# Kernel optimization log

Measured on AMD Instinct MI355X. Metric: run time of the kernel, lower is better.

Reference implementation:

```python
import jax, jax.numpy as jnp
import numpy as np

KERNEL = 7
PAD = 3
STRIDE = 1
DIL = 1
HEADS = 8
OUT_CH = 256


def _unfold(x, k, pad, stride, dil):
    # x: (B, C, H, W) -> (B, C*k*k, Ho, Wo); channel ordering (C, kh, kw),
    # matching torch.nn.Unfold's channel-major layout.
    return jax.lax.conv_general_dilated_patches(
        x, filter_shape=(k, k), window_strides=(stride, stride),
        padding=((pad, pad), (pad, pad)), rhs_dilation=(dil, dil))


def _conv1x1(x, w, b):
    # 1x1 conv == per-pixel matmul. w: (O, C), b: (O,)
    return jnp.einsum('bchw,oc->bohw', x, w) + b[None, :, None, None]


def setup_inputs() -> dict:
    key = jax.random.key(0)
    ks = jax.random.split(key, 11)
    B, C, H, W = 2, 256, 64, 64
    f = lambda k, sh: jax.random.normal(k, sh, dtype=jnp.float32)
    ws = 1.0 / np.sqrt(C).astype(np.float32)
    return dict(
        queries=f(ks[0], (B, C, H, W)),
        keys=f(ks[1], (B, C, H, W)),
        values=f(ks[2], (B, C, H, W)),
        wq=f(ks[3], (OUT_CH, C)) * ws, bq=f(ks[4], (OUT_CH,)) * 0.01,
        wk=f(ks[5], (OUT_CH, C)) * ws, bk=f(ks[6], (OUT_CH,)) * 0.01,
        wv=f(ks[7], (OUT_CH, C)) * ws, bv=f(ks[8], (OUT_CH,)) * 0.01,
        wo=f(ks[9], (OUT_CH, OUT_CH)) * ws, bo=f(ks[10], (OUT_CH,)) * 0.01,
    )


def reference(queries, keys, values, wq, bq, wk, bk, wv, bv, wo, bo):
    B = values.shape[0]
    d = OUT_CH // HEADS
    K2 = KERNEL * KERNEL
    q = _conv1x1(queries, wq, bq)
    k = _conv1x1(keys, wk, bk)
    v = _conv1x1(values, wv, bv)
    # query 'unfold' with kernel 1, stride STRIDE == strided subsample
    q = q[:, :, ::STRIDE, ::STRIDE]
    Ho, Wo = q.shape[-2], q.shape[-1]
    L = Ho * Wo
    q = q.reshape(B, HEADS, d, L)                                  # (B,h,d,L)
    kp = _unfold(k, KERNEL, PAD, STRIDE, DIL).reshape(B, HEADS, d, K2, L)
    vp = _unfold(v, KERNEL, PAD, STRIDE, DIL).reshape(B, HEADS, d, K2, L)
    scale = jnp.float32(1.0 / np.sqrt(OUT_CH))                     # note: sqrt(out_channels), per source
    attn = jnp.einsum('bhdl,bhdkl->bhlk', q, kp) * scale           # (B,h,L,K2)
    attn = jax.nn.softmax(attn, axis=-1)
    out = jnp.einsum('bhdkl,bhlk->bhdl', vp, attn)                 # (B,h,d,L)
    out = out.reshape(B, OUT_CH, Ho, Wo)
    return _conv1x1(out, wo, bo)
```

## Files before the change

kernel.cpp:

```cpp
#include <hip/hip_runtime.h>
#include <hip/hip_fp16.h>
#include <math.h>

#define B_ 2
#define C_ 256
#define H_ 64
#define W_ 64
#define L_ 4096
#define HEADS_ 8
#define DH_ 32
#define K_ 7
#define PAD_ 3
#define K2_ 49
#define PW_ 70
#define PPIX_ 4900
#define NPP_ 4
#define PADT4_ ((size_t)B_*HEADS_*NPP_*PPIX_)
#define WS_STR 72
#define KVW_ (NPP_*K_*PW_)

typedef _Float16 f16x8 __attribute__((ext_vector_type(8)));
typedef _Float16 h2    __attribute__((ext_vector_type(2)));
typedef float    f32x4 __attribute__((ext_vector_type(4)));

__device__ inline h2 u2h(unsigned u) { union { unsigned u; h2 h; } c; c.u = u; return c.h; }
__device__ inline h2 cvt2h(float a, float b) {
    auto r = __builtin_amdgcn_cvt_pkrtz(a, b);
    union { decltype(r) s; h2 d; } c; c.s = r; return c.d;
}
__device__ inline unsigned pkh(float a, float b) {
    union { h2 h; unsigned u; } c; c.h = cvt2h(a, b); return c.u;
}

__global__ __launch_bounds__(256) void prep(
    const float* __restrict__ wq, const float* __restrict__ wk,
    const float* __restrict__ wv, const float* __restrict__ wo,
    unsigned* __restrict__ wb)
{
    int idx = blockIdx.x*256 + threadIdx.x;
    const float* src = (idx < 32768) ? wq : (idx < 65536) ? wk : (idx < 98304) ? wv : wo;
    int off = (idx & 32767) * 2;
    wb[idx] = pkh(src[off], src[off+1]);
}

__global__ __launch_bounds__(256) void qkv_mfma(
    const float* __restrict__ q_in, const float* __restrict__ k_in, const float* __restrict__ v_in,
    const unsigned* __restrict__ wb,
    const float* __restrict__ bq, const float* __restrict__ bk, const float* __restrict__ bv,
    uint2* __restrict__ qt_u2, uint2* __restrict__ kt_u2, uint2* __restrict__ vt_u2,
    uint4* __restrict__ kt_u4, uint4* __restrict__ vt_u4)
{
    const int z = blockIdx.z;
    const int tid = threadIdx.x;

    if (z == 6) {
        const int flat = blockIdx.x + 64*blockIdx.y;
        const uint4 zz = make_uint4(0u,0u,0u,0u);
        for (int e = flat*256 + tid; e < 64*804; e += 128*256) {
            int pl = e / 804;
            int c  = e - pl*804;
            int py, px;
            if (c < 210)      { py = c/70;            px = c%70; }
            else if (c < 420) { int c2 = c-210; py = 67 + c2/70; px = c2%70; }
            else              { int c2 = c-420; py = 3 + c2/6; int j = c2%6; px = (j<3) ? j : 64+j; }
            size_t idx = (size_t)pl*PPIX_ + (size_t)py*PW_ + px;
            kt_u4[idx] = zz;
            vt_u4[idx] = zz;
        }
        return;
    }

    const int which = z >> 1;
    const int b = z & 1;
    const float* X = (which==0) ? q_in : (which==1 ? k_in : v_in);
    const unsigned* wbp = wb + which*32768;
    const float* bias = (which==0) ? bq : (which==1 ? bk : bv);

    const int y    = blockIdx.x;
    const int l0   = y * 64;
    const int o_t0 = blockIdx.y * 128;
    const int lane = tid & 63, wave = tid >> 6;
    const int orow = lane & 15, kgrp = lane >> 4;

    __shared__ _Float16 Ws[128*WS_STR];
    __shared__ _Float16 Xs[64*WS_STR];

    f32x4 acc[2][4] = {};

    for (int ch = 0; ch < 4; ++ch) {
        const int c0 = ch*64;
        #pragma unroll
        for (int i = 0; i < 4; ++i) {
            int flat = i*256 + tid;
            int o    = flat >> 3;
            int c16  = flat & 7;
            uint4 v = *reinterpret_cast<const uint4*>(wbp + (size_t)(o_t0 + o)*128 + ch*32 + c16*4);
            *reinterpret_cast<uint4*>(&Ws[o*WS_STR + c16*8]) = v;
        }
        #pragma unroll
        for (int i = 0; i < 2; ++i) {
            int c_loc = (tid>>4)*2 + i*32;
            int l4    = (tid&15)*4;
            float4 x0 = *reinterpret_cast<const float4*>(&X[(size_t)(b*C_ + c0 + c_loc    )*L_ + l0 + l4]);
            float4 x1 = *reinterpret_cast<const float4*>(&X[(size_t)(b*C_ + c0 + c_loc + 1)*L_ + l0 + l4]);
            *reinterpret_cast<unsigned*>(&Xs[(l4+0)*WS_STR + c_loc]) = pkh(x0.x, x1.x);
            *reinterpret_cast<unsigned*>(&Xs[(l4+1)*WS_STR + c_loc]) = pkh(x0.y, x1.y);
            *reinterpret_cast<unsigned*>(&Xs[(l4+2)*WS_STR + c_loc]) = pkh(x0.z, x1.z);
            *reinterpret_cast<unsigned*>(&Xs[(l4+3)*WS_STR + c_loc]) = pkh(x0.w, x1.w);
        }
        __syncthreads();
        #pragma unroll
        for (int kk = 0; kk < 2; ++kk) {
            f16x8 af[2], bfr[4];
            #pragma unroll
            for (int fo = 0; fo < 2; ++fo)
                af[fo] = *reinterpret_cast<const f16x8*>(&Ws[(wave*32 + fo*16 + orow)*WS_STR + kk*32 + kgrp*8]);
            #pragma unroll
            for (int fn = 0; fn < 4; ++fn)
                bfr[fn] = *reinterpret_cast<const f16x8*>(&Xs[(fn*16 + orow)*WS_STR + kk*32 + kgrp*8]);
            #pragma unroll
            for (int fo = 0; fo < 2; ++fo)
                #pragma unroll
                for (int fn = 0; fn < 4; ++fn)
                    acc[fo][fn] = __builtin_amdgcn_mfma_f32_16x16x32_f16(af[fo], bfr[fn], acc[fo][fn], 0, 0, 0);
        }
        __syncthreads();
    }

    #pragma unroll
    for (int fo = 0; fo < 2; ++fo) {
        const int og = o_t0 + wave*32 + fo*16 + kgrp*4;
        const float4 b4 = *reinterpret_cast<const float4*>(&bias[og]);
        const size_t pp = (size_t)(b*32 + (og >> 3));
        const int half = (og >> 2) & 1;
        #pragma unroll
        for (int fn = 0; fn < 4; ++fn) {
            const int xl = fn*16 + orow;
            uint2 r = make_uint2(pkh(acc[fo][fn][0] + b4.x, acc[fo][fn][1] + b4.y),
                                 pkh(acc[fo][fn][2] + b4.z, acc[fo][fn][3] + b4.w));
            if (which == 0) {
                qt_u2[(pp*L_ + l0 + xl)*2 + half] = r;
            } else {
                uint2* dst = (which==1) ? kt_u2 : vt_u2;
                dst[(pp*PPIX_ + (size_t)(y+PAD_)*PW_ + (xl+PAD_))*2 + half] = r;
            }
        }
    }
}

__global__ __launch_bounds__(256) void local_attn(
    uint4* __restrict__ qt, const uint4* __restrict__ kt, const uint4* __restrict__ vt)
{
    const int tid = threadIdx.x;
    const int w = tid >> 6, x = tid & 63;
    const int bid = blockIdx.x;
    const int plane = bid & 15;
    const int y = bid >> 4;

    const uint4* kb = kt + (size_t)plane*NPP_*PPIX_;
    const uint4* vb = vt + (size_t)plane*NPP_*PPIX_;
    uint4* qpl = qt + (size_t)plane*NPP_*L_;

    __shared__ uint4 KV[KVW_];
    __shared__ float S[K2_][64];

    const float scale = 0.0625f;

    uint4 qu[NPP_];
    #pragma unroll
    for (int pp=0; pp<NPP_; ++pp) qu[pp] = qpl[(size_t)pp*L_ + y*W_ + x];

    #pragma unroll
    for (int i = 0; i < 8; ++i) {
        int e = tid + i*256;
        if (e < KVW_) {
            int pp = e / (K_*PW_);
            int rem = e - pp*(K_*PW_);
            int r = rem / PW_, xp = rem - r*PW_;
            KV[e] = kb[(size_t)pp*PPIX_ + (size_t)(y + r)*PW_ + xp];
        }
    }
    __syncthreads();

    float lg[2][K_] = {};
    #pragma unroll
    for (int pp=0; pp<NPP_; ++pp) {
        const h2 q0 = u2h(qu[pp].x), q1 = u2h(qu[pp].y), q2 = u2h(qu[pp].z), q3 = u2h(qu[pp].w);
        #pragma unroll
        for (int rr=0; rr<2; ++rr) {
            const int r = w + rr*4;
            if (r > 6) continue;
            const uint4* row = &KV[(pp*K_ + r)*PW_ + x];
            #pragma unroll
            for (int kx=0; kx<K_; ++kx) {
                uint4 kk = row[kx];
                float d = lg[rr][kx];
                d = __builtin_amdgcn_fdot2(q0, u2h(kk.x), d, false);
                d = __builtin_amdgcn_fdot2(q1, u2h(kk.y), d, false);
                d = __builtin_amdgcn_fdot2(q2, u2h(kk.z), d, false);
                d = __builtin_amdgcn_fdot2(q3, u2h(kk.w), d, false);
                lg[rr][kx] = d;
            }
        }
    }
    #pragma unroll
    for (int rr=0; rr<2; ++rr) {
        const int r = w + rr*4;
        if (r <= 6) {
            #pragma unroll
            for (int kx=0; kx<K_; ++kx) S[r*K_+kx][x] = __expf(lg[rr][kx]*scale);
        }
    }
    __syncthreads();

    #pragma unroll
    for (int i = 0; i < 8; ++i) {
        int e = tid + i*256;
        if (e < KVW_) {
            int pp = e / (K_*PW_);
            int rem = e - pp*(K_*PW_);
            int r = rem / PW_, xp = rem - r*PW_;
            KV[e] = vb[(size_t)pp*PPIX_ + (size_t)(y + r)*PW_ + xp];
        }
    }

    float sum = 0.f;
    #pragma unroll
    for (int i=0;i<K2_;++i) sum += S[i][x];
    const float inv = 1.0f/sum;
    __syncthreads();

    float4 a0 = make_float4(0.f,0.f,0.f,0.f);
    float4 a1 = make_float4(0.f,0.f,0.f,0.f);
    #pragma unroll
    for (int r=0; r<K_; ++r) {
        const uint4* row = &KV[(w*K_ + r)*PW_ + x];
        h2 ra0 = (h2)0, ra1 = (h2)0, rb0 = (h2)0, rb1 = (h2)0;
        #pragma unroll
        for (int kx=0; kx<K_; ++kx) {
            const float p = S[r*K_+kx][x];
            const h2 p2 = cvt2h(p, p);
            uint4 u = row[kx];
            ra0 += p2 * u2h(u.x);
            ra1 += p2 * u2h(u.y);
            rb0 += p2 * u2h(u.z);
            rb1 += p2 * u2h(u.w);
        }
        a0.x += (float)ra0[0]; a0.y += (float)ra0[1];
        a0.z += (float)ra1[0]; a0.w += (float)ra1[1];
        a1.x += (float)rb0[0]; a1.y += (float)rb0[1];
        a1.z += (float)rb1[0]; a1.w += (float)rb1[1];
    }
    qpl[(size_t)w*L_ + y*W_ + x] = make_uint4(pkh(a0.x*inv, a0.y*inv), pkh(a0.z*inv, a0.w*inv),
                                              pkh(a1.x*inv, a1.y*inv), pkh(a1.z*inv, a1.w*inv));
}

__global__ __launch_bounds__(256) void out_mfma(
    const uint4* __restrict__ qt, const unsigned* __restrict__ wb,
    const float* __restrict__ bo, float* __restrict__ out)
{
    const int b    = blockIdx.z;
    const int l0   = blockIdx.x * 64;
    const int o_t0 = blockIdx.y * 64;
    const unsigned* wbp = wb + 3*32768;
    const int tid  = threadIdx.x;
    const int lane = tid & 63, wave = tid >> 6;
    const int orow = lane & 15, kgrp = lane >> 4;

    __shared__ _Float16 Ws[64*WS_STR];
    __shared__ _Float16 Xs[64*WS_STR];

    f32x4 acc[4] = {};
    const int cq  = tid >> 6;
    const int lst = tid & 63;

    for (int ch = 0; ch < 4; ++ch) {
        const int c0 = ch*64;
        #pragma unroll
        for (int i = 0; i < 2; ++i) {
            int flat = i*256 + tid;
            int o    = flat >> 3;
            int c16  = flat & 7;
            uint4 v = *reinterpret_cast<const uint4*>(wbp + (size_t)(o_t0 + o)*128 + ch*32 + c16*4);
            *reinterpret_cast<uint4*>(&Ws[o*WS_STR + c16*8]) = v;
        }
        #pragma unroll
        for (int i = 0; i < 2; ++i) {
            int c8 = i*4 + cq;
            uint4 v = qt[((size_t)b*32 + (c0>>3) + c8)*L_ + l0 + lst];
            *reinterpret_cast<uint4*>(&Xs[lst*WS_STR + c8*8]) = v;
        }
        __syncthreads();
        #pragma unroll
        for (int kk = 0; kk < 2; ++kk) {
            f16x8 af, bfr[4];
            af = *reinterpret_cast<const f16x8*>(&Ws[(wave*16 + orow)*WS_STR + kk*32 + kgrp*8]);
            #pragma unroll
            for (int fn = 0; fn < 4; ++fn)
                bfr[fn] = *reinterpret_cast<const f16x8*>(&Xs[(fn*16 + orow)*WS_STR + kk*32 + kgrp*8]);
            #pragma unroll
            for (int fn = 0; fn < 4; ++fn)
                acc[fn] = __builtin_amdgcn_mfma_f32_16x16x32_f16(af, bfr[fn], acc[fn], 0, 0, 0);
        }
        __syncthreads();
    }

    {
        const int o_base = o_t0 + wave*16 + kgrp*4;
        #pragma unroll
        for (int fn = 0; fn < 4; ++fn) {
            const int xl = fn*16 + orow;
            #pragma unroll
            for (int r = 0; r < 4; ++r)
                out[(size_t)(b*C_ + o_base + r)*L_ + l0 + xl] = acc[fn][r] + bo[o_base + r];
        }
    }
}

extern "C" void kernel_launch(void* const* d_in, const int* in_sizes, int n_in,
                              void* d_out, int out_size, void* d_ws, size_t ws_size,
                              hipStream_t stream) {
    const float* queries = (const float*)d_in[0];
    const float* keys    = (const float*)d_in[1];
    const float* values  = (const float*)d_in[2];
    const float* wq = (const float*)d_in[3];
    const float* bq = (const float*)d_in[4];
    const float* wk = (const float*)d_in[5];
    const float* bk = (const float*)d_in[6];
    const float* wv = (const float*)d_in[7];
    const float* bv = (const float*)d_in[8];
    const float* wo = (const float*)d_in[9];
    const float* bo = (const float*)d_in[10];
    float* out = (float*)d_out;

    uint4* qt = (uint4*)d_ws;
    uint4* kt = qt + (size_t)B_*HEADS_*NPP_*L_;
    uint4* vt = kt + PADT4_;
    unsigned* wb = (unsigned*)(vt + PADT4_);

    prep<<<512, 256, 0, stream>>>(wq, wk, wv, wo, wb);
    qkv_mfma<<<dim3(64, 2, 7), 256, 0, stream>>>(queries, keys, values, wb, bq, bk, bv,
                                                 (uint2*)qt, (uint2*)kt, (uint2*)vt, kt, vt);
    local_attn<<<1024, 256, 0, stream>>>(qt, kt, vt);
    out_mfma<<<dim3(64, 4, 2), 256, 0, stream>>>(qt, wb, bo, out);
}
```

Measured before the change: 46.37 us.

## Process two output rows per block in local attention to reuse K/V halo rows

Each local_attn block now handles two adjacent output rows, loading 8 K/V rows instead of 7 per row and sharing them across both rows, which cuts global K/V loads and LDS fill work roughly in half per output. The grid is halved to 512 blocks, softmax probabilities are stored as fp16 in shared memory, and row sums come from per-wave partial sums instead of a 49-element reread. The costs are fewer blocks for occupancy, more registers for two sets of logits and accumulators, and slightly lower precision in the stored probabilities.

```diff
diff --git a/kernel.cpp b/kernel.cpp
--- a/kernel.cpp
+++ b/kernel.cpp
@@ -17,7 +17,7 @@
 #define NPP_ 4
 #define PADT4_ ((size_t)B_*HEADS_*NPP_*PPIX_)
 #define WS_STR 72
-#define KVW_ (NPP_*K_*PW_)
+#define KVW2_ (NPP_*8*PW_)
 
 typedef _Float16 f16x8 __attribute__((ext_vector_type(8)));
 typedef _Float16 h2    __attribute__((ext_vector_type(2)));
@@ -31,6 +31,7 @@
 __device__ inline unsigned pkh(float a, float b) {
     union { h2 h; unsigned u; } c; c.h = cvt2h(a, b); return c.u;
 }
+__device__ inline h2 dup2(_Float16 v) { h2 r; r[0] = v; r[1] = v; return r; }
 
 __global__ __launch_bounds__(256) void prep(
     const float* __restrict__ wq, const float* __restrict__ wk,
@@ -155,104 +156,150 @@
     const int w = tid >> 6, x = tid & 63;
     const int bid = blockIdx.x;
     const int plane = bid & 15;
-    const int y = bid >> 4;
+    const int y0 = (bid >> 4) * 2;
 
     const uint4* kb = kt + (size_t)plane*NPP_*PPIX_;
     const uint4* vb = vt + (size_t)plane*NPP_*PPIX_;
     uint4* qpl = qt + (size_t)plane*NPP_*L_;
 
-    __shared__ uint4 KV[KVW_];
-    __shared__ float S[K2_][64];
+    __shared__ uint4 KV[KVW2_];
+    __shared__ _Float16 S0[K2_][64];
+    __shared__ _Float16 S1[K2_][64];
+    __shared__ float PS[2][4][64];
 
     const float scale = 0.0625f;
 
-    uint4 qu[NPP_];
-    #pragma unroll
-    for (int pp=0; pp<NPP_; ++pp) qu[pp] = qpl[(size_t)pp*L_ + y*W_ + x];
-
-    #pragma unroll
-    for (int i = 0; i < 8; ++i) {
+    uint4 qa[NPP_], qb[NPP_];
+    #pragma unroll
+    for (int pp=0; pp<NPP_; ++pp) {
+        qa[pp] = qpl[(size_t)pp*L_ + (y0  )*W_ + x];
+        qb[pp] = qpl[(size_t)pp*L_ + (y0+1)*W_ + x];
+    }
+
+    #pragma unroll
+    for (int i = 0; i < 9; ++i) {
         int e = tid + i*256;
-        if (e < KVW_) {
-            int pp = e / (K_*PW_);
-            int rem = e - pp*(K_*PW_);
+        if (e < KVW2_) {
+            int pp = e / (8*PW_);
+            int rem = e - pp*(8*PW_);
             int r = rem / PW_, xp = rem - r*PW_;
-            KV[e] = kb[(size_t)pp*PPIX_ + (size_t)(y + r)*PW_ + xp];
+            KV[e] = kb[(size_t)pp*PPIX_ + (size_t)(y0 + r)*PW_ + xp];
         }
     }
     __syncthreads();
 
-    float lg[2][K_] = {};
+    float lgA[2][K_] = {};
+    float lgB[2][K_] = {};
     #pragma unroll
     for (int pp=0; pp<NPP_; ++pp) {
-        const h2 q0 = u2h(qu[pp].x), q1 = u2h(qu[pp].y), q2 = u2h(qu[pp].z), q3 = u2h(qu[pp].w);
+        const h2 qa0 = u2h(qa[pp].x), qa1 = u2h(qa[pp].y), qa2 = u2h(qa[pp].z), qa3 = u2h(qa[pp].w);
+        const h2 qb0 = u2h(qb[pp].x), qb1 = u2h(qb[pp].y), qb2 = u2h(qb[pp].z), qb3 = u2h(qb[pp].w);
         #pragma unroll
         for (int rr=0; rr<2; ++rr) {
-            const int r = w + rr*4;
-            if (r > 6) continue;
-            const uint4* row = &KV[(pp*K_ + r)*PW_ + x];
+            const int r = 2*w + rr;
+            const uint4* row = &KV[(pp*8 + r)*PW_ + x];
             #pragma unroll
             for (int kx=0; kx<K_; ++kx) {
                 uint4 kk = row[kx];
-                float d = lg[rr][kx];
-                d = __builtin_amdgcn_fdot2(q0, u2h(kk.x), d, false);
-                d = __builtin_amdgcn_fdot2(q1, u2h(kk.y), d, false);
-                d = __builtin_amdgcn_fdot2(q2, u2h(kk.z), d, false);
-                d = __builtin_amdgcn_fdot2(q3, u2h(kk.w), d, false);
-                lg[rr][kx] = d;
-            }
-        }
-    }
+                h2 k0 = u2h(kk.x), k1 = u2h(kk.y), k2 = u2h(kk.z), k3 = u2h(kk.w);
+                if (r < 7) {
+                    float d = lgA[rr][kx];
+                    d = __builtin_amdgcn_fdot2(qa0, k0, d, false);
+                    d = __builtin_amdgcn_fdot2(qa1, k1, d, false);
+                    d = __builtin_amdgcn_fdot2(qa2, k2, d, false);
+                    d = __builtin_amdgcn_fdot2(qa3, k3, d, false);
+                    lgA[rr][kx] = d;
+                }
+                if (r > 0) {
+                    float d = lgB[rr][kx];
+                    d = __builtin_amdgcn_fdot2(qb0, k0, d, false);
+                    d = __builtin_amdgcn_fdot2(qb1, k1, d, false);
+                    d = __builtin_amdgcn_fdot2(qb2, k2, d, false);
+                    d = __builtin_amdgcn_fdot2(qb3, k3, d, false);
+                    lgB[rr][kx] = d;
+                }
+            }
+        }
+    }
+    float psA = 0.f, psB = 0.f;
     #pragma unroll
     for (int rr=0; rr<2; ++rr) {
-        const int r = w + rr*4;
-        if (r <= 6) {
-            #pragma unroll
-            for (int kx=0; kx<K_; ++kx) S[r*K_+kx][x] = __expf(lg[rr][kx]*scale);
-        }
-    }
+        const int r = 2*w + rr;
+        if (r < 7) {
+            #pragma unroll
+            for (int kx=0; kx<K_; ++kx) {
+                float p = __expf(lgA[rr][kx]*scale);
+                psA += p;
+                S0[r*K_+kx][x] = (_Float16)p;
+            }
+        }
+        if (r > 0) {
+            #pragma unroll
+            for (int kx=0; kx<K_; ++kx) {
+                float p = __expf(lgB[rr][kx]*scale);
+                psB += p;
+                S1[(r-1)*K_+kx][x] = (_Float16)p;
+            }
+        }
+    }
+    PS[0][w][x] = psA;
+    PS[1][w][x] = psB;
     __syncthreads();
 
     #pragma unroll
-    for (int i = 0; i < 8; ++i) {
+    for (int i = 0; i < 9; ++i) {
         int e = tid + i*256;
-        if (e < KVW_) {
-            int pp = e / (K_*PW_);
-            int rem = e - pp*(K_*PW_);
+        if (e < KVW2_) {
+            int pp = e / (8*PW_);
+            int rem = e - pp*(8*PW_);
             int r = rem / PW_, xp = rem - r*PW_;
-            KV[e] = vb[(size_t)pp*PPIX_ + (size_t)(y + r)*PW_ + xp];
-        }
-    }
-
-    float sum = 0.f;
-    #pragma unroll
-    for (int i=0;i<K2_;++i) sum += S[i][x];
-    const float inv = 1.0f/sum;
+            KV[e] = vb[(size_t)pp*PPIX_ + (size_t)(y0 + r)*PW_ + xp];
+        }
+    }
+
+    const float inv0 = 1.0f/(PS[0][0][x] + PS[0][1][x] + PS[0][2][x] + PS[0][3][x]);
+    const float inv1 = 1.0f/(PS[1][0][x] + PS[1][1][x] + PS[1][2][x] + PS[1][3][x]);
     __syncthreads();
 
     float4 a0 = make_float4(0.f,0.f,0.f,0.f);
+    float4 a0h = make_float4(0.f,0.f,0.f,0.f);
     float4 a1 = make_float4(0.f,0.f,0.f,0.f);
-    #pragma unroll
-    for (int r=0; r<K_; ++r) {
-        const uint4* row = &KV[(w*K_ + r)*PW_ + x];
-        h2 ra0 = (h2)0, ra1 = (h2)0, rb0 = (h2)0, rb1 = (h2)0;
+    float4 a1h = make_float4(0.f,0.f,0.f,0.f);
+    #pragma unroll
+    for (int r8=0; r8<8; ++r8) {
+        const uint4* row = &KV[(w*8 + r8)*PW_ + x];
+        h2 pa0=(h2)0, pa1=(h2)0, pa2=(h2)0, pa3=(h2)0;
+        h2 pb0=(h2)0, pb1=(h2)0, pb2=(h2)0, pb3=(h2)0;
         #pragma unroll
         for (int kx=0; kx<K_; ++kx) {
-            const float p = S[r*K_+kx][x];
-            const h2 p2 = cvt2h(p, p);
             uint4 u = row[kx];
-            ra0 += p2 * u2h(u.x);
-            ra1 += p2 * u2h(u.y);
-            rb0 += p2 * u2h(u.z);
-            rb1 += p2 * u2h(u.w);
-        }
-        a0.x += (float)ra0[0]; a0.y += (float)ra0[1];
-        a0.z += (float)ra1[0]; a0.w += (float)ra1[1];
-        a1.x += (float)rb0[0]; a1.y += (float)rb0[1];
-        a1.z += (float)rb1[0]; a1.w += (float)rb1[1];
-    }
-    qpl[(size_t)w*L_ + y*W_ + x] = make_uint4(pkh(a0.x*inv, a0.y*inv), pkh(a0.z*inv, a0.w*inv),
-                                              pkh(a1.x*inv, a1.y*inv), pkh(a1.z*inv, a1.w*inv));
+            h2 v0 = u2h(u.x), v1 = u2h(u.y), v2 = u2h(u.z), v3 = u2h(u.w);
+            if (r8 < 7) {
+                h2 p2 = dup2(S0[r8*K_+kx][x]);
+                pa0 += p2*v0; pa1 += p2*v1; pa2 += p2*v2; pa3 += p2*v3;
+            }
+            if (r8 > 0) {
+                h2 p2 = dup2(S1[(r8-1)*K_+kx][x]);
+                pb0 += p2*v0; pb1 += p2*v1; pb2 += p2*v2; pb3 += p2*v3;
+            }
+        }
+        if (r8 < 7) {
+            a0.x  += (float)pa0[0]; a0.y  += (float)pa0[1];
+            a0.z  += (float)pa1[0]; a0.w  += (float)pa1[1];
+            a0h.x += (float)pa2[0]; a0h.y += (float)pa2[1];
+            a0h.z += (float)pa3[0]; a0h.w += (float)pa3[1];
+        }
+        if (r8 > 0) {
+            a1.x  += (float)pb0[0]; a1.y  += (float)pb0[1];
+            a1.z  += (float)pb1[0]; a1.w  += (float)pb1[1];
+            a1h.x += (float)pb2[0]; a1h.y += (float)pb2[1];
+            a1h.z += (float)pb3[0]; a1h.w += (float)pb3[1];
+        }
+    }
+    qpl[(size_t)w*L_ + (y0  )*W_ + x] = make_uint4(pkh(a0.x*inv0, a0.y*inv0), pkh(a0.z*inv0, a0.w*inv0),
+                                                   pkh(a0h.x*inv0, a0h.y*inv0), pkh(a0h.z*inv0, a0h.w*inv0));
+    qpl[(size_t)w*L_ + (y0+1)*W_ + x] = make_uint4(pkh(a1.x*inv1, a1.y*inv1), pkh(a1.z*inv1, a1.w*inv1),
+                                                   pkh(a1h.x*inv1, a1h.y*inv1), pkh(a1h.z*inv1, a1h.w*inv1));
 }
 
 __global__ __launch_bounds__(256) void out_mfma(
@@ -341,6 +388,6 @@
     prep<<<512, 256, 0, stream>>>(wq, wk, wv, wo, wb);
     qkv_mfma<<<dim3(64, 2, 7), 256, 0, stream>>>(queries, keys, values, wb, bq, bk, bv,
                                                  (uint2*)qt, (uint2*)kt, (uint2*)vt, kt, vt);
-    local_attn<<<1024, 256, 0, stream>>>(qt, kt, vt);
+    local_attn<<<512, 256, 0, stream>>>(qt, kt, vt);
     out_mfma<<<dim3(64, 4, 2), 256, 0, stream>>>(qt, wb, bo, out);
 }
```

Measured after the change: 48.17 us. +3.9%, slower.
